# Kernel tuning notes

Hardware: AMD Instinct MI355X
Metric: run time of the kernel (lower is better)

## Reference

```python
import jax, jax.numpy as jnp
import numpy as np

EMBED, HEADS, LEVELS, POINTS, MLP = 256, 8, 3, 4, 4
SHAPES = [(60, 80), (30, 40), (15, 20)]  # (H, W) per level


def layer_norm(x, g, b):
    m = jnp.mean(x, -1, keepdims=True)
    v = jnp.mean((x - m) ** 2, -1, keepdims=True)
    return (x - m) * jax.lax.rsqrt(v + 1e-5) * g + b


def _bilinear(v, H, W, gx, gy):
    # v: [B,h,H*W,dh]; gx,gy: [B,h,Nq,P] absolute pixel coords (grid_sample align_corners=False, zero padding)
    x0 = jnp.floor(gx); y0 = jnp.floor(gy)
    wx = gx - x0; wy = gy - y0

    def g(xi, yi):
        valid = ((xi >= 0) & (xi < W) & (yi >= 0) & (yi < H)).astype(v.dtype)
        idx = jnp.clip(yi, 0, H - 1) * W + jnp.clip(xi, 0, W - 1)
        B, h, Nq, P = idx.shape
        out = jnp.take_along_axis(v, idx.reshape(B, h, Nq * P)[..., None], axis=2)
        return out.reshape(B, h, Nq, P, -1) * valid[..., None]

    x0i = x0.astype(jnp.int32); y0i = y0.astype(jnp.int32)
    return (g(x0i, y0i) * ((1 - wx) * (1 - wy))[..., None]
            + g(x0i + 1, y0i) * (wx * (1 - wy))[..., None]
            + g(x0i, y0i + 1) * ((1 - wx) * wy)[..., None]
            + g(x0i + 1, y0i + 1) * (wx * wy)[..., None])


def setup_inputs() -> dict:
    key = jax.random.key(0)
    ks = jax.random.split(key, 16)
    B, Nq, C = 2, 8192, EMBED
    Nv = sum(h * w for h, w in SHAPES)
    s = 0.02
    d = {
        'query': jax.random.normal(ks[0], (B, Nq, C), jnp.float32),
        'value': jax.random.normal(ks[1], (B, Nv, C), jnp.float32),
        'query_pos': jax.random.normal(ks[2], (B, Nq, C), jnp.float32),
        'ref_pts': jax.random.uniform(ks[3], (B, Nq, LEVELS, 2), jnp.float32),
        'spatial_shapes': jnp.array(SHAPES, jnp.int32),
        'level_start_index': jnp.array(np.cumsum([0] + [h * w for h, w in SHAPES[:-1]]), jnp.int32),
        'g1': jnp.ones((C,), jnp.float32), 'b1': jnp.zeros((C,), jnp.float32),
        'Wo': s * jax.random.normal(ks[4], (C, HEADS * LEVELS * POINTS * 2), jnp.float32),
        'bo': jnp.zeros((HEADS * LEVELS * POINTS * 2,), jnp.float32),
        'Wa': s * jax.random.normal(ks[5], (C, HEADS * LEVELS * POINTS), jnp.float32),
        'ba': jnp.zeros((HEADS * LEVELS * POINTS,), jnp.float32),
        'Wv': s * jax.random.normal(ks[6], (C, C), jnp.float32), 'bv': jnp.zeros((C,), jnp.float32),
        'Wp': s * jax.random.normal(ks[7], (C, C), jnp.float32), 'bp': jnp.zeros((C,), jnp.float32),
        'g2': jnp.ones((C,), jnp.float32), 'b2': jnp.zeros((C,), jnp.float32),
        'Wf1': s * jax.random.normal(ks[8], (C, MLP * C), jnp.float32), 'bf1': jnp.zeros((MLP * C,), jnp.float32),
        'Wf2': s * jax.random.normal(ks[9], (MLP * C, C), jnp.float32), 'bf2': jnp.zeros((C,), jnp.float32),
    }
    return d


def reference(query, value, query_pos, ref_pts, spatial_shapes, level_start_index,
              g1, b1, Wo, bo, Wa, ba, Wv, bv, Wp, bp, g2, b2, Wf1, bf1, Wf2, bf2):
    B, Nq, C = query.shape
    dh = C // HEADS
    shapes = np.asarray(spatial_shapes).tolist()
    starts = np.asarray(level_start_index).tolist()

    qn = layer_norm(query, g1, b1)           # pre-norm
    qa = qn + query_pos                       # positional embedding inside attn
    offs = (qa @ Wo + bo).reshape(B, Nq, HEADS, LEVELS, POINTS, 2)
    aw = jax.nn.softmax((qa @ Wa + ba).reshape(B, Nq, HEADS, LEVELS * POINTS), -1)
    aw = aw.reshape(B, Nq, HEADS, LEVELS, POINTS)
    v = (value @ Wv + bv).reshape(B, -1, HEADS, dh).transpose(0, 2, 1, 3)  # [B,h,Nv,dh]

    # offset_normalizer = (W, H) per level
    norm = jnp.array([[w, h] for h, w in shapes], jnp.float32)
    loc = ref_pts[:, :, None, :, None, :] + offs / norm[None, None, None, :, None, :]

    out = jnp.zeros((B, Nq, HEADS, dh), query.dtype)
    for l, (H, W) in enumerate(shapes):
        vl = jax.lax.dynamic_slice_in_dim(v, starts[l], H * W, axis=2)
        gl = loc[:, :, :, l].transpose(0, 2, 1, 3, 4)   # [B,h,Nq,P,2]
        gx = gl[..., 0] * W - 0.5
        gy = gl[..., 1] * H - 0.5
        sampled = _bilinear(vl, H, W, gx, gy)            # [B,h,Nq,P,dh]
        out = out + jnp.einsum('bhqpd,bqhp->bqhd', sampled, aw[:, :, :, l])

    attn = out.reshape(B, Nq, C) @ Wp + bp + qn          # output proj + mmcv internal residual (identity=norm1(query))
    q = query + attn                                     # layer residual
    q2 = layer_norm(q, g2, b2)
    return q + (jax.nn.gelu(q2 @ Wf1 + bf1, approximate=False) @ Wf2 + bf2)
```

## Files before the change

kernel.cpp:

```cpp
#include <hip/hip_runtime.h>
#include <math.h>


typedef short short8 __attribute__((ext_vector_type(8)));
typedef short s16x4 __attribute__((ext_vector_type(4)));
typedef __bf16 bf16x8 __attribute__((ext_vector_type(8)));
typedef float f32x4 __attribute__((ext_vector_type(4)));

__device__ __forceinline__ short f2b(float f) {
  unsigned u = __builtin_bit_cast(unsigned, f);
  u += 0x7fffu + ((u >> 16) & 1u);
  return (short)(u >> 16);
}
__device__ __forceinline__ float b2f(short s) {
  unsigned u = ((unsigned)(unsigned short)s) << 16;
  return __builtin_bit_cast(float, u);
}
__device__ __forceinline__ void b8f(short8 s, float* f) {
  const uint4 u = __builtin_bit_cast(uint4, s);
  f[0] = __builtin_bit_cast(float, u.x << 16);
  f[1] = __builtin_bit_cast(float, u.x & 0xffff0000u);
  f[2] = __builtin_bit_cast(float, u.y << 16);
  f[3] = __builtin_bit_cast(float, u.y & 0xffff0000u);
  f[4] = __builtin_bit_cast(float, u.z << 16);
  f[5] = __builtin_bit_cast(float, u.z & 0xffff0000u);
  f[6] = __builtin_bit_cast(float, u.w << 16);
  f[7] = __builtin_bit_cast(float, u.w & 0xffff0000u);
}

__device__ __forceinline__ f32x4 mfma16(short8 a, short8 b, f32x4 c) {
  return __builtin_amdgcn_mfma_f32_16x16x32_bf16(
      __builtin_bit_cast(bf16x8, a), __builtin_bit_cast(bf16x8, b), c, 0, 0, 0);
}

typedef __attribute__((address_space(3))) unsigned int lds_u32;
typedef const __attribute__((address_space(1))) unsigned int glb_u32;
__device__ __forceinline__ void glds16(const void* g, void* l) {
  __builtin_amdgcn_global_load_lds((glb_u32*)g, (lds_u32*)l, 16, 0, 0);
}

__device__ __forceinline__ float gelu1(float v) {
  return 0.5f * v * (1.f + erff(v * 0.70710678118654752f));
}

template <int EPI>
__device__ __forceinline__ void gemm64_core(
    int bx, int by,
    const short* __restrict__ A, const short* __restrict__ Bt,
    const float* __restrict__ bias, const float* __restrict__ bias2,
    const void* __restrict__ add1,
    void* __restrict__ Cout, int M, int Nreal, int ldc, int K, char* smem)
{
  short* sA = (short*)smem;
  short* sB = sA + 4096;
  float* sf = (float*)smem;

  const int t = threadIdx.x;
  const int wave = t >> 6, lane = t & 63;
  const int quad = lane >> 4, l16 = lane & 15;
  const int wm = (wave & 1) * 32, wn = (wave >> 1) * 64;
  const int m0 = by * 64, n0 = bx * 128;

  f32x4 acc[2][4];
#pragma unroll
  for (int i = 0; i < 2; i++)
#pragma unroll
    for (int j = 0; j < 4; j++) acc[i][j] = (f32x4){0.f, 0.f, 0.f, 0.f};

  const int srow = lane >> 3, pos = lane & 7;
  const int chunk = (pos + srow) & 7;
  const short* gA = A + (size_t)(m0 + wave * 16 + srow) * K + chunk * 8;
  const short* gB = Bt + (size_t)(n0 + wave * 32 + srow) * K + chunk * 8;

  const int nk = K >> 6;
  for (int kt = 0; kt < nk; ++kt) {
    if (kt) __syncthreads();
    const int ko = kt * 64;
#pragma unroll
    for (int g = 0; g < 2; ++g)
      glds16(gA + ko + (size_t)(g * 8) * K, sA + (wave * 16 + g * 8) * 64);
#pragma unroll
    for (int g = 0; g < 4; ++g)
      glds16(gB + ko + (size_t)(g * 8) * K, sB + (wave * 32 + g * 8) * 64);
    __syncthreads();
#pragma unroll
    for (int kk = 0; kk < 2; ++kk) {
      short8 af[2], bf[4];
      const int c = kk * 4 + quad;
#pragma unroll
      for (int i = 0; i < 2; i++) {
        const int lrA = wm + i * 16 + l16;
        af[i] = *(const short8*)&sA[lrA * 64 + ((c - lrA) & 7) * 8];
      }
#pragma unroll
      for (int j = 0; j < 4; j++) {
        const int lrB = wn + j * 16 + l16;
        bf[j] = *(const short8*)&sB[lrB * 64 + ((c - lrB) & 7) * 8];
      }
#pragma unroll
      for (int i = 0; i < 2; i++)
#pragma unroll
        for (int j = 0; j < 4; j++) acc[i][j] = mfma16(bf[j], af[i], acc[i][j]);
    }
  }
  __syncthreads();

#pragma unroll
  for (int b = 0; b < 2; ++b) {
    if (wm == b * 32) {
#pragma unroll
      for (int i = 0; i < 2; ++i) {
        const int rr = i * 16 + l16;
#pragma unroll
        for (int j = 0; j < 4; ++j)
          *(f32x4*)&sf[rr * 132 + wn + quad * 4 + j * 16] = acc[i][j];
      }
    }
    __syncthreads();
#pragma unroll
    for (int r2 = 0; r2 < 4; ++r2) {
      const int fidx = r2 * 1024 + t * 4;
      const int row = fidx >> 7, col = fidx & 127;
      const int gm = m0 + b * 32 + row;
      const int cc = n0 + col;
      if (gm < M && cc < Nreal) {
        const float4 v = *(const float4*)&sf[row * 132 + col];
        float4 bb;
        if (EPI == 4) bb = (cc < 192) ? *(const float4*)(bias + cc)
                                      : *(const float4*)(bias2 + cc - 192);
        else bb = *(const float4*)(bias + cc);
        float v0 = v.x + bb.x, v1 = v.y + bb.y, v2 = v.z + bb.z, v3 = v.w + bb.w;
        s16x4 o; o.x = f2b(v0); o.y = f2b(v1); o.z = f2b(v2); o.w = f2b(v3);
        *(s16x4*)((short*)Cout + (size_t)gm * ldc + cc) = o;
      }
    }
    __syncthreads();
  }
}

__global__ __launch_bounds__(256) void gemm_oa_v(
    const short* __restrict__ qa, const short* __restrict__ wt_oa,
    const float* __restrict__ bo, const float* __restrict__ ba,
    short* __restrict__ oabuf,
    const short* __restrict__ valbf, const short* __restrict__ wt_v,
    const float* __restrict__ bv, short* __restrict__ vproj)
{
  __shared__ __align__(16) char smem[24576];
  const int idx = blockIdx.x;
  if (idx < 768) {
    gemm64_core<4>(idx % 3, idx / 3, qa, wt_oa, bo, ba, nullptr,
                   oabuf, 16384, 288, 288, 256, smem);
  } else {
    const int r = idx - 768;
    gemm64_core<5>(r % 2, r / 2, valbf, wt_v, bv, nullptr, nullptr,
                   vproj, 12600, 256, 256, 256, smem);
  }
}

__global__ __launch_bounds__(256) void gemm_wp_ln2(
    const short* __restrict__ A, const short* __restrict__ Bt,
    const float* __restrict__ bias,
    const short* __restrict__ qnb, const float* __restrict__ query,
    const float* __restrict__ g2, const float* __restrict__ b2v,
    float* __restrict__ qbuf, short* __restrict__ q2)
{
  __shared__ __align__(16) char smem[36864];
  short* sA = (short*)smem;
  short* sB = sA + 2048;
  float* sf = (float*)smem;

  const int t = threadIdx.x;
  const int wave = t >> 6, lane = t & 63;
  const int quad = lane >> 4, l16 = lane & 15;
  const int wm = (wave & 1) * 16, wn = (wave >> 1) * 128;
  const int m0 = blockIdx.x * 32;
  const int K = 256;

  f32x4 acc[8];
#pragma unroll
  for (int j = 0; j < 8; j++) acc[j] = (f32x4){0.f, 0.f, 0.f, 0.f};

  const int srow = lane >> 3, pos = lane & 7;
  const int chunk = (pos + srow) & 7;
  const short* gA = A + (size_t)(m0 + wave * 8 + srow) * K + chunk * 8;
  const short* gB = Bt + (size_t)(wave * 64 + srow) * K + chunk * 8;

  for (int kt = 0; kt < 4; ++kt) {
    if (kt) __syncthreads();
    const int ko = kt * 64;
    glds16(gA + ko, sA + (wave * 8) * 64);
#pragma unroll
    for (int g = 0; g < 8; ++g)
      glds16(gB + ko + (size_t)(g * 8) * K, sB + (wave * 64 + g * 8) * 64);
    __syncthreads();
#pragma unroll
    for (int kk = 0; kk < 2; ++kk) {
      const int c = kk * 4 + quad;
      const int lrA = wm + l16;
      const short8 af = *(const short8*)&sA[lrA * 64 + ((c - lrA) & 7) * 8];
      short8 bf[8];
#pragma unroll
      for (int j = 0; j < 8; j++) {
        const int lrB = wn + j * 16 + l16;
        bf[j] = *(const short8*)&sB[lrB * 64 + ((c - lrB) & 7) * 8];
      }
#pragma unroll
      for (int j = 0; j < 8; j++) acc[j] = mfma16(bf[j], af, acc[j]);
    }
  }
  __syncthreads();

#pragma unroll
  for (int j = 0; j < 8; j++)
    *(f32x4*)&sf[(wm + l16) * 260 + wn + j * 16 + quad * 4] = acc[j];
  __syncthreads();

  const float4 bb   = *(const float4*)(bias + lane * 4);
  const float4 gv   = *(const float4*)(g2 + lane * 4);
  const float4 b2f4 = *(const float4*)(b2v + lane * 4);
#pragma unroll
  for (int rr = 0; rr < 8; ++rr) {
    const int row = wave * 8 + rr;
    const int gm = m0 + row;
    const float4 a = *(const float4*)&sf[row * 260 + lane * 4];
    const s16x4 qn = *(const s16x4*)(qnb + (size_t)gm * 256 + lane * 4);
    const float4 qv = *(const float4*)(query + (size_t)gm * 256 + lane * 4);
    float q0 = a.x + bb.x + b2f(qn.x) + qv.x;
    float q1 = a.y + bb.y + b2f(qn.y) + qv.y;
    float q2f = a.z + bb.z + b2f(qn.z) + qv.z;
    float q3 = a.w + bb.w + b2f(qn.w) + qv.w;
    float s = q0 + q1 + q2f + q3;
#pragma unroll
    for (int o = 32; o; o >>= 1) s += __shfl_xor(s, o);
    const float mean = s * (1.f / 256.f);
    const float d0 = q0 - mean, d1 = q1 - mean, d2 = q2f - mean, d3 = q3 - mean;
    float ss = d0 * d0 + d1 * d1 + d2 * d2 + d3 * d3;
#pragma unroll
    for (int o = 32; o; o >>= 1) ss += __shfl_xor(ss, o);
    const float inv = rsqrtf(ss * (1.f / 256.f) + 1e-5f);
    *(float4*)(qbuf + (size_t)gm * 256 + lane * 4) = make_float4(q0, q1, q2f, q3);
    s16x4 o2;
    o2.x = f2b(d0 * inv * gv.x + b2f4.x);
    o2.y = f2b(d1 * inv * gv.y + b2f4.y);
    o2.z = f2b(d2 * inv * gv.z + b2f4.z);
    o2.w = f2b(d3 * inv * gv.w + b2f4.w);
    *(s16x4*)(q2 + (size_t)gm * 256 + lane * 4) = o2;
  }
}

__global__ __launch_bounds__(1024, 4) void fused_mlp(
    const short* __restrict__ q2,
    const short* __restrict__ wf1,
    const float* __restrict__ b1v,
    const short* __restrict__ wf2,
    const float* __restrict__ b2v,
    const float* __restrict__ qbuf,
    float* __restrict__ outp)
{
  __shared__ __align__(16) char smem[147456];
  short* H  = (short*)smem;
  short* sA = (short*)(smem + 131072);
  float* sf = (float*)smem;

  const int t = threadIdx.x;
  const int w = t >> 6, lane = t & 63;
  const int quad = lane >> 4, l16 = lane & 15;
  const int m0 = blockIdx.x * 64;

  f32x4 acc[4][4];
#pragma unroll
  for (int i = 0; i < 4; i++)
#pragma unroll
    for (int j = 0; j < 4; j++) acc[i][j] = (f32x4){0.f, 0.f, 0.f, 0.f};

  for (int ap = 0; ap < 2; ++ap) {
    if (ap) __syncthreads();
    {
      const int row = t >> 4, pp = t & 15;
      const int cl = (pp & ~7) | ((pp + row) & 7);
      glds16(q2 + (size_t)(m0 + row) * 256 + (size_t)(ap * 16 + cl) * 8,
             sA + (size_t)w * 512);
    }
    __syncthreads();
#pragma unroll
    for (int kk = 0; kk < 4; ++kk) {
      const int cl = kk * 4 + quad;
      const int cg = ap * 16 + cl;
      short8 bfr[4], afr[4];
#pragma unroll
      for (int j = 0; j < 4; ++j) {
        const int n1 = w * 4 + j;
        bfr[j] = *(const short8*)(wf1 + ((size_t)n1 * 32 + cg) * 128 + l16 * 8);
      }
#pragma unroll
      for (int i = 0; i < 4; ++i) {
        const int r = i * 16 + l16;
        const int pos = (cl & ~7) | ((cl - r) & 7);
        afr[i] = *(const short8*)(sA + r * 128 + pos * 8);
      }
#pragma unroll
      for (int i = 0; i < 4; ++i)
#pragma unroll
        for (int j = 0; j < 4; ++j) acc[i][j] = mfma16(bfr[j], afr[i], acc[i][j]);
    }
  }
#pragma unroll
  for (int j = 0; j < 4; ++j) {
    const int colb = w * 64 + j * 16 + quad * 4;
    const float4 bb = *(const float4*)(b1v + colb);
    const int c = colb >> 3;
#pragma unroll
    for (int i = 0; i < 4; ++i) {
      const int r = i * 16 + l16;
      const int pos = (c & ~7) | ((c - r) & 7);
      s16x4 o;
      o.x = f2b(gelu1(acc[i][j].x + bb.x));
      o.y = f2b(gelu1(acc[i][j].y + bb.y));
      o.z = f2b(gelu1(acc[i][j].z + bb.z));
      o.w = f2b(gelu1(acc[i][j].w + bb.w));
      *(s16x4*)(H + r * 1024 + pos * 8 + (colb & 7)) = o;
    }
  }
  __syncthreads();

  float4 qv[4];
#pragma unroll
  for (int rep = 0; rep < 4; ++rep) {
    const int fidx = rep * 4096 + t * 4;
    qv[rep] = *(const float4*)(qbuf + (size_t)(m0 + (fidx >> 8)) * 256 + (fidx & 255));
  }

  const int wm2 = w >> 3, wn8 = w & 7;
  f32x4 acc2[2][2];
#pragma unroll
  for (int i = 0; i < 2; i++)
#pragma unroll
    for (int j = 0; j < 2; j++) acc2[i][j] = (f32x4){0.f, 0.f, 0.f, 0.f};

#pragma unroll 4
  for (int kk = 0; kk < 32; ++kk) {
    const int c = kk * 4 + quad;
    short8 bfr[2], afr[2];
#pragma unroll
    for (int j = 0; j < 2; ++j) {
      const int n1 = wn8 * 2 + j;
      bfr[j] = *(const short8*)(wf2 + ((size_t)n1 * 128 + c) * 128 + l16 * 8);
    }
#pragma unroll
    for (int i = 0; i < 2; ++i) {
      const int r = wm2 * 32 + i * 16 + l16;
      const int pos = (c & ~7) | ((c - r) & 7);
      afr[i] = *(const short8*)(H + r * 1024 + pos * 8);
    }
#pragma unroll
    for (int i = 0; i < 2; ++i)
#pragma unroll
      for (int j = 0; j < 2; ++j) acc2[i][j] = mfma16(bfr[j], afr[i], acc2[i][j]);
  }
  __syncthreads();

#pragma unroll
  for (int i = 0; i < 2; ++i)
#pragma unroll
    for (int j = 0; j < 2; ++j)
      *(f32x4*)&sf[(wm2 * 32 + i * 16 + l16) * 260 + wn8 * 32 + j * 16 + quad * 4] =
          acc2[i][j];
  __syncthreads();

#pragma unroll
  for (int rep = 0; rep < 4; ++rep) {
    const int fidx = rep * 4096 + t * 4;
    const int row = fidx >> 8, col = fidx & 255;
    const int gm = m0 + row;
    const float4 v  = *(const float4*)&sf[row * 260 + col];
    const float4 bb = *(const float4*)(b2v + col);
    *(float4*)(outp + (size_t)gm * 256 + col) =
        make_float4(v.x + bb.x + qv[rep].x, v.y + bb.y + qv[rep].y,
                    v.z + bb.z + qv[rep].z, v.w + bb.w + qv[rep].w);
  }
}

__global__ __launch_bounds__(256) void prep_all(
    const float* __restrict__ Wo, const float* __restrict__ Wa,
    const float* __restrict__ Wv, const float* __restrict__ Wp,
    const float* __restrict__ Wf1, const float* __restrict__ Wf2,
    short* __restrict__ t_oa, short* __restrict__ t_v, short* __restrict__ t_p,
    short* __restrict__ t_f1, short* __restrict__ t_f2,
    const float* __restrict__ value, short* __restrict__ valbf,
    const float* __restrict__ query, const float* __restrict__ query_pos,
    const float* __restrict__ g1, const float* __restrict__ b1,
    short* __restrict__ qnb, short* __restrict__ qa)
{
  __shared__ float tile[32][33];
  const int t = threadIdx.x;
  const int blk = blockIdx.x;

  if (blk < 1792) {
    const int bxa = blk & 255, bya = blk >> 8;
    int K, N, noff; const float* src; short* dst;
    switch (bya) {
      case 0: src = Wo;      dst = t_oa; K = 256;  N = 192;  noff = 0;   break;
      case 1: src = Wa;      dst = t_oa; K = 256;  N = 96;   noff = 192; break;
      case 2: src = nullptr; dst = t_oa; K = 256;  N = 96;   noff = 288; break;
      case 3: src = Wv;      dst = t_v;  K = 256;  N = 256;  noff = 0;   break;
      case 4: src = Wp;      dst = t_p;  K = 256;  N = 256;  noff = 0;   break;
      case 5: src = Wf1;     dst = t_f1; K = 256;  N = 1024; noff = 0;   break;
      default: src = Wf2;    dst = t_f2; K = 1024; N = 256;  noff = 0;   break;
    }
    const bool fragpack = (bya >= 5);
    const int tilesK = K >> 5;
    const int nt = tilesK * (N >> 5);
    if (bxa >= nt) return;
    const int tk = bxa % tilesK, tn = bxa / tilesK;
    const int k0 = tk * 32, n0 = tn * 32;
    const int r = t >> 3, c4 = (t & 7) * 4;
    float4 v = make_float4(0.f, 0.f, 0.f, 0.f);
    if (src) v = *(const float4*)(src + (size_t)(k0 + r) * N + n0 + c4);
    tile[r][c4] = v.x; tile[r][c4 + 1] = v.y; tile[r][c4 + 2] = v.z; tile[r][c4 + 3] = v.w;
    __syncthreads();
    const int nn = t >> 3, kc = (t & 7) * 4;
    s16x4 o;
    o.x = f2b(tile[kc][nn]); o.y = f2b(tile[kc + 1][nn]);
    o.z = f2b(tile[kc + 2][nn]); o.w = f2b(tile[kc + 3][nn]);
    if (fragpack) {
      const int n = n0 + nn, k = k0 + kc;
      *(s16x4*)(dst + ((size_t)(n >> 4) * (K >> 3) + (k >> 3)) * 128 +
                (n & 15) * 8 + (k & 7)) = o;
    } else {
      *(s16x4*)(dst + (size_t)(noff + n0 + nn) * K + k0 + kc) = o;
    }
  } else if (blk < 1792 + 3169) {
    const int i = ((blk - 1792) * 256 + t) * 4;
    if (i >= 12672 * 256) return;
    s16x4 o = (s16x4){0, 0, 0, 0};
    if (i < 12600 * 256) {
      float4 v = *(const float4*)(value + i);
      o.x = f2b(v.x); o.y = f2b(v.y); o.z = f2b(v.z); o.w = f2b(v.w);
    }
    *(s16x4*)(valbf + i) = o;
  } else {
    const int row  = (blk - 4961) * 4 + (t >> 6);
    const int lane = t & 63;
    const float4 v = ((const float4*)(query + (size_t)row * 256))[lane];
    float s = v.x + v.y + v.z + v.w;
#pragma unroll
    for (int o = 32; o; o >>= 1) s += __shfl_xor(s, o);
    const float mean = s * (1.f / 256.f);
    const float dx = v.x - mean, dy = v.y - mean, dz = v.z - mean, dw = v.w - mean;
    float s2 = dx * dx + dy * dy + dz * dz + dw * dw;
#pragma unroll
    for (int o = 32; o; o >>= 1) s2 += __shfl_xor(s2, o);
    const float inv = rsqrtf(s2 * (1.f / 256.f) + 1e-5f);
    const float4 gv = ((const float4*)g1)[lane];
    const float4 bv = ((const float4*)b1)[lane];
    const float4 o1 = make_float4(dx * inv * gv.x + bv.x, dy * inv * gv.y + bv.y,
                                  dz * inv * gv.z + bv.z, dw * inv * gv.w + bv.w);
    s16x4 ob; ob.x = f2b(o1.x); ob.y = f2b(o1.y); ob.z = f2b(o1.z); ob.w = f2b(o1.w);
    ((s16x4*)(qnb + (size_t)row * 256))[lane] = ob;
    const float4 pv = ((const float4*)(query_pos + (size_t)row * 256))[lane];
    s16x4 op;
    op.x = f2b(o1.x + pv.x); op.y = f2b(o1.y + pv.y);
    op.z = f2b(o1.z + pv.z); op.w = f2b(o1.w + pv.w);
    ((s16x4*)(qa + (size_t)row * 256))[lane] = op;
  }
}

__global__ __launch_bounds__(256) void deform_fused(
    const short* __restrict__ vproj, const short* __restrict__ oa,
    const float* __restrict__ refp, short* __restrict__ out)
{
  __shared__ int4 sIdx[768];
  __shared__ s16x4 sW[768];
  const int t = threadIdx.x;

  if (t < 64) {
    const int row = blockIdx.x * 8 + (t >> 3), h = t & 7;
    const short* oarow = oa + (size_t)row * 288;
    float off[24];
    {
      const short8* op = (const short8*)(oarow + h * 24);
      b8f(op[0], off); b8f(op[1], off + 8); b8f(op[2], off + 16);
    }
    float lg[12];
    {
      const s16x4* ap = (const s16x4*)(oarow + 192 + h * 12);
#pragma unroll
      for (int i = 0; i < 3; i++) {
        const s16x4 v = ap[i];
        lg[i * 4] = b2f(v.x); lg[i * 4 + 1] = b2f(v.y);
        lg[i * 4 + 2] = b2f(v.z); lg[i * 4 + 3] = b2f(v.w);
      }
    }
    const float* rp = refp + (size_t)row * 6;
    const float Rx[3] = {rp[0], rp[2], rp[4]}, Ry[3] = {rp[1], rp[3], rp[5]};
    float mx = lg[0];
#pragma unroll
    for (int i = 1; i < 12; i++) mx = fmaxf(mx, lg[i]);
    float sum = 0.f;
#pragma unroll
    for (int i = 0; i < 12; i++) { lg[i] = __expf(lg[i] - mx); sum += lg[i]; }
    const float inv = 1.f / sum;
    const int b = row >> 13;
    const int Hs[3] = {60, 30, 15}, Ws[3] = {80, 40, 20}, St[3] = {0, 4800, 6000};
#pragma unroll
    for (int p = 0; p < 12; p++) {
      const int l = p >> 2;
      const int W = Ws[l], H = Hs[l];
      const float gx = Rx[l] * W + off[p * 2]     - 0.5f;
      const float gy = Ry[l] * H + off[p * 2 + 1] - 0.5f;
      const float x0f = floorf(gx), y0f = floorf(gy);
      const float wx = gx - x0f, wy = gy - y0f;
      const int x0 = (int)x0f, y0 = (int)y0f;
      const float aw = lg[p] * inv;
      float cw[4] = {(1.f - wx) * (1.f - wy), wx * (1.f - wy),
                     (1.f - wx) * wy, wx * wy};
      const int base = b * 6300 + St[l];
      int ci[4];
#pragma unroll
      for (int k = 0; k < 4; k++) {
        const int xx = x0 + (k & 1), yy = y0 + (k >> 1);
        const bool valid = (xx >= 0) & (xx < W) & (yy >= 0) & (yy < H);
        const int xc = min(max(xx, 0), W - 1);
        const int yc = min(max(yy, 0), H - 1);
        ci[k] = ((base + yc * W + xc) << 8) + h * 32;
        cw[k] = valid ? cw[k] * aw : 0.f;
      }
      sIdx[t * 12 + p] = make_int4(ci[0], ci[1], ci[2], ci[3]);
      s16x4 wv; wv.x = f2b(cw[0]); wv.y = f2b(cw[1]); wv.z = f2b(cw[2]); wv.w = f2b(cw[3]);
      sW[t * 12 + p] = wv;
    }
  }
  __syncthreads();

  const int lu = t >> 2, c4 = (t & 3) * 8;
  float acc[8];
#pragma unroll
  for (int i = 0; i < 8; i++) acc[i] = 0.f;
#pragma unroll 2
  for (int p = 0; p < 12; p++) {
    const int4 idx = sIdx[lu * 12 + p];
    const s16x4 wb = sW[lu * 12 + p];
    const float w0 = b2f(wb.x), w1 = b2f(wb.y), w2 = b2f(wb.z), w3 = b2f(wb.w);
    const short8 v0 = *(const short8*)(vproj + idx.x + c4);
    const short8 v1 = *(const short8*)(vproj + idx.y + c4);
    const short8 v2 = *(const short8*)(vproj + idx.z + c4);
    const short8 v3 = *(const short8*)(vproj + idx.w + c4);
    float f0[8], f1[8], f2[8], f3[8];
    b8f(v0, f0); b8f(v1, f1); b8f(v2, f2); b8f(v3, f3);
#pragma unroll
    for (int j = 0; j < 8; j++)
      acc[j] += w0 * f0[j] + w1 * f1[j] + w2 * f2[j] + w3 * f3[j];
  }
  short8 o;
#pragma unroll
  for (int j = 0; j < 8; j++) o[j] = f2b(acc[j]);
  *(short8*)(out + (size_t)(blockIdx.x * 256 + t) * 8) = o;
}

extern "C" void kernel_launch(void* const* d_in, const int* in_sizes, int n_in,
                              void* d_out, int out_size, void* d_ws, size_t ws_size,
                              hipStream_t stream)
{
  const float* query     = (const float*)d_in[0];
  const float* value     = (const float*)d_in[1];
  const float* query_pos = (const float*)d_in[2];
  const float* ref_pts   = (const float*)d_in[3];
  const float* g1  = (const float*)d_in[6];
  const float* b1  = (const float*)d_in[7];
  const float* Wo  = (const float*)d_in[8];
  const float* bo  = (const float*)d_in[9];
  const float* Wa  = (const float*)d_in[10];
  const float* ba  = (const float*)d_in[11];
  const float* Wv  = (const float*)d_in[12];
  const float* bv  = (const float*)d_in[13];
  const float* Wp  = (const float*)d_in[14];
  const float* bp  = (const float*)d_in[15];
  const float* g2  = (const float*)d_in[16];
  const float* b2  = (const float*)d_in[17];
  const float* Wf1 = (const float*)d_in[18];
  const float* bf1 = (const float*)d_in[19];
  const float* Wf2 = (const float*)d_in[20];
  const float* bf2 = (const float*)d_in[21];

  char* ws = (char*)d_ws;
  short* wt_oa   = (short*)(ws + 0);
  short* wt_v    = (short*)(ws + 196608);
  short* wt_p    = (short*)(ws + 327680);
  short* wt_f1   = (short*)(ws + 458752);
  short* wt_f2   = (short*)(ws + 983040);
  short* qnb     = (short*)(ws + 1507328);
  short* qa      = (short*)(ws + 18284544);
  short* oabuf   = (short*)(ws + 26673152);
  short* vproj   = (short*)(ws + 45547520);
  short* sampled = (short*)(ws + 51998720);
  float* qbuf    = (float*)(ws + 60387328);
  short* valbf   = (short*)(ws + 77164544);
  short* q2      = qa;
  float* outp = (float*)d_out;

  prep_all<<<9057, 256, 0, stream>>>(Wo, Wa, Wv, Wp, Wf1, Wf2,
                                     wt_oa, wt_v, wt_p, wt_f1, wt_f2,
                                     value, valbf, query, query_pos,
                                     g1, b1, qnb, qa);
  gemm_oa_v<<<1162, 256, 0, stream>>>(qa, wt_oa, bo, ba, oabuf,
                                      valbf, wt_v, bv, vproj);
  deform_fused<<<2048, 256, 0, stream>>>(vproj, oabuf, ref_pts, sampled);
  gemm_wp_ln2<<<512, 256, 0, stream>>>(sampled, wt_p, bp, qnb, query,
                                       g2, b2, qbuf, q2);
  fused_mlp<<<256, 1024, 0, stream>>>(q2, wt_f1, bf1, wt_f2, bf2, qbuf, outp);
}
```

Measured before the change: 210.6 us.

## Fuse output projection and LayerNorm2 into the MLP kernel

Merges the Wp projection + residual + LayerNorm2 kernel into the fused MLP kernel, so the q2 and qbuf intermediates stay on chip (in LDS and registers) and are never written to or reread from global memory. The Wp weights are now fragment-packed so they can be read directly from global memory. The hidden layer is processed in two halves of 512 columns to shrink LDS use, which adds extra synchronisation and an inner loop. The 1024-thread blocks now also do the Wp GEMM, and that adds work per block.

Measured after the change: 207.5 us. Within noise of the previous version (-1.5%).

```diff
diff --git a/kernel.cpp b/kernel.cpp
--- a/kernel.cpp
+++ b/kernel.cpp
@@ -48,7 +48,6 @@
     int bx, int by,
     const short* __restrict__ A, const short* __restrict__ Bt,
     const float* __restrict__ bias, const float* __restrict__ bias2,
-    const void* __restrict__ add1,
     void* __restrict__ Cout, int M, int Nreal, int ldc, int K, char* smem)
 {
   short* sA = (short*)smem;
@@ -148,214 +147,194 @@
   __shared__ __align__(16) char smem[24576];
   const int idx = blockIdx.x;
   if (idx < 768) {
-    gemm64_core<4>(idx % 3, idx / 3, qa, wt_oa, bo, ba, nullptr,
+    gemm64_core<4>(idx % 3, idx / 3, qa, wt_oa, bo, ba,
                    oabuf, 16384, 288, 288, 256, smem);
   } else {
     const int r = idx - 768;
-    gemm64_core<5>(r % 2, r / 2, valbf, wt_v, bv, nullptr, nullptr,
+    gemm64_core<5>(r % 2, r / 2, valbf, wt_v, bv, nullptr,
                    vproj, 12600, 256, 256, 256, smem);
   }
 }
 
-__global__ __launch_bounds__(256) void gemm_wp_ln2(
-    const short* __restrict__ A, const short* __restrict__ Bt,
-    const float* __restrict__ bias,
-    const short* __restrict__ qnb, const float* __restrict__ query,
+__global__ __launch_bounds__(1024, 4) void wp_mlp(
+    const short* __restrict__ sampled,
+    const short* __restrict__ wtp,
+    const float* __restrict__ bp,
+    const short* __restrict__ qnb,
+    const float* __restrict__ query,
     const float* __restrict__ g2, const float* __restrict__ b2v,
-    float* __restrict__ qbuf, short* __restrict__ q2)
-{
-  __shared__ __align__(16) char smem[36864];
-  short* sA = (short*)smem;
-  short* sB = sA + 2048;
-  float* sf = (float*)smem;
-
-  const int t = threadIdx.x;
-  const int wave = t >> 6, lane = t & 63;
-  const int quad = lane >> 4, l16 = lane & 15;
-  const int wm = (wave & 1) * 16, wn = (wave >> 1) * 128;
-  const int m0 = blockIdx.x * 32;
-  const int K = 256;
-
-  f32x4 acc[8];
-#pragma unroll
-  for (int j = 0; j < 8; j++) acc[j] = (f32x4){0.f, 0.f, 0.f, 0.f};
-
-  const int srow = lane >> 3, pos = lane & 7;
-  const int chunk = (pos + srow) & 7;
-  const short* gA = A + (size_t)(m0 + wave * 8 + srow) * K + chunk * 8;
-  const short* gB = Bt + (size_t)(wave * 64 + srow) * K + chunk * 8;
-
-  for (int kt = 0; kt < 4; ++kt) {
-    if (kt) __syncthreads();
-    const int ko = kt * 64;
-    glds16(gA + ko, sA + (wave * 8) * 64);
-#pragma unroll
-    for (int g = 0; g < 8; ++g)
-      glds16(gB + ko + (size_t)(g * 8) * K, sB + (wave * 64 + g * 8) * 64);
-    __syncthreads();
-#pragma unroll
-    for (int kk = 0; kk < 2; ++kk) {
-      const int c = kk * 4 + quad;
-      const int lrA = wm + l16;
-      const short8 af = *(const short8*)&sA[lrA * 64 + ((c - lrA) & 7) * 8];
-      short8 bf[8];
-#pragma unroll
-      for (int j = 0; j < 8; j++) {
-        const int lrB = wn + j * 16 + l16;
-        bf[j] = *(const short8*)&sB[lrB * 64 + ((c - lrB) & 7) * 8];
-      }
-#pragma unroll
-      for (int j = 0; j < 8; j++) acc[j] = mfma16(bf[j], af, acc[j]);
-    }
-  }
-  __syncthreads();
-
-#pragma unroll
-  for (int j = 0; j < 8; j++)
-    *(f32x4*)&sf[(wm + l16) * 260 + wn + j * 16 + quad * 4] = acc[j];
-  __syncthreads();
-
-  const float4 bb   = *(const float4*)(bias + lane * 4);
-  const float4 gv   = *(const float4*)(g2 + lane * 4);
-  const float4 b2f4 = *(const float4*)(b2v + lane * 4);
-#pragma unroll
-  for (int rr = 0; rr < 8; ++rr) {
-    const int row = wave * 8 + rr;
-    const int gm = m0 + row;
-    const float4 a = *(const float4*)&sf[row * 260 + lane * 4];
-    const s16x4 qn = *(const s16x4*)(qnb + (size_t)gm * 256 + lane * 4);
-    const float4 qv = *(const float4*)(query + (size_t)gm * 256 + lane * 4);
-    float q0 = a.x + bb.x + b2f(qn.x) + qv.x;
-    float q1 = a.y + bb.y + b2f(qn.y) + qv.y;
-    float q2f = a.z + bb.z + b2f(qn.z) + qv.z;
-    float q3 = a.w + bb.w + b2f(qn.w) + qv.w;
-    float s = q0 + q1 + q2f + q3;
-#pragma unroll
-    for (int o = 32; o; o >>= 1) s += __shfl_xor(s, o);
-    const float mean = s * (1.f / 256.f);
-    const float d0 = q0 - mean, d1 = q1 - mean, d2 = q2f - mean, d3 = q3 - mean;
-    float ss = d0 * d0 + d1 * d1 + d2 * d2 + d3 * d3;
-#pragma unroll
-    for (int o = 32; o; o >>= 1) ss += __shfl_xor(ss, o);
-    const float inv = rsqrtf(ss * (1.f / 256.f) + 1e-5f);
-    *(float4*)(qbuf + (size_t)gm * 256 + lane * 4) = make_float4(q0, q1, q2f, q3);
-    s16x4 o2;
-    o2.x = f2b(d0 * inv * gv.x + b2f4.x);
-    o2.y = f2b(d1 * inv * gv.y + b2f4.y);
-    o2.z = f2b(d2 * inv * gv.z + b2f4.z);
-    o2.w = f2b(d3 * inv * gv.w + b2f4.w);
-    *(s16x4*)(q2 + (size_t)gm * 256 + lane * 4) = o2;
-  }
-}
-
-__global__ __launch_bounds__(1024, 4) void fused_mlp(
-    const short* __restrict__ q2,
     const short* __restrict__ wf1,
     const float* __restrict__ b1v,
     const short* __restrict__ wf2,
-    const float* __restrict__ b2v,
-    const float* __restrict__ qbuf,
+    const float* __restrict__ bf2v,
     float* __restrict__ outp)
 {
-  __shared__ __align__(16) char smem[147456];
+  __shared__ __align__(16) char smem[99328];
+  float* sf = (float*)smem;
   short* H  = (short*)smem;
-  short* sA = (short*)(smem + 131072);
-  float* sf = (float*)smem;
+  short* RA = (short*)(smem + 66560);
 
   const int t = threadIdx.x;
   const int w = t >> 6, lane = t & 63;
   const int quad = lane >> 4, l16 = lane & 15;
+  const int wm2 = w >> 3, wn8 = w & 7;
   const int m0 = blockIdx.x * 64;
 
-  f32x4 acc[4][4];
-#pragma unroll
-  for (int i = 0; i < 4; i++)
-#pragma unroll
-    for (int j = 0; j < 4; j++) acc[i][j] = (f32x4){0.f, 0.f, 0.f, 0.f};
-
-  for (int ap = 0; ap < 2; ++ap) {
-    if (ap) __syncthreads();
-    {
-      const int row = t >> 4, pp = t & 15;
-      const int cl = (pp & ~7) | ((pp + row) & 7);
-      glds16(q2 + (size_t)(m0 + row) * 256 + (size_t)(ap * 16 + cl) * 8,
-             sA + (size_t)w * 512);
-    }
-    __syncthreads();
-#pragma unroll
-    for (int kk = 0; kk < 4; ++kk) {
-      const int cl = kk * 4 + quad;
-      const int cg = ap * 16 + cl;
-      short8 bfr[4], afr[4];
-#pragma unroll
-      for (int j = 0; j < 4; ++j) {
-        const int n1 = w * 4 + j;
+#pragma unroll
+  for (int q = 0; q < 2; ++q) {
+    const int row = q * 32 + w * 2 + (lane >> 5);
+    const int pos = lane & 31;
+    const int cl = (pos & ~7) | ((pos + row) & 7);
+    glds16(sampled + (size_t)(m0 + row) * 256 + cl * 8, RA + q * 8192 + w * 512);
+  }
+  __syncthreads();
+
+  {
+    f32x4 accp[2][2];
+#pragma unroll
+    for (int i = 0; i < 2; i++)
+#pragma unroll
+      for (int j = 0; j < 2; j++) accp[i][j] = (f32x4){0.f, 0.f, 0.f, 0.f};
+#pragma unroll
+    for (int kk = 0; kk < 8; ++kk) {
+      const int c = kk * 4 + quad;
+      short8 bfr[2], afr[2];
+#pragma unroll
+      for (int j = 0; j < 2; ++j) {
+        const int n1 = wn8 * 2 + j;
+        bfr[j] = *(const short8*)(wtp + ((size_t)n1 * 32 + c) * 128 + l16 * 8);
+      }
+#pragma unroll
+      for (int i = 0; i < 2; ++i) {
+        const int r = wm2 * 32 + i * 16 + l16;
+        const int pos = (c & ~7) | ((c - r) & 7);
+        afr[i] = *(const short8*)(RA + r * 256 + pos * 8);
+      }
+#pragma unroll
+      for (int i = 0; i < 2; ++i)
+#pragma unroll
+        for (int j = 0; j < 2; ++j) accp[i][j] = mfma16(bfr[j], afr[i], accp[i][j]);
+    }
+#pragma unroll
+    for (int i = 0; i < 2; ++i)
+#pragma unroll
+      for (int j = 0; j < 2; ++j)
+        *(f32x4*)&sf[(wm2 * 32 + i * 16 + l16) * 260 + wn8 * 32 + j * 16 + quad * 4] =
+            accp[i][j];
+  }
+  __syncthreads();
+
+  float4 qb[4];
+  {
+    const float4 bbp  = *(const float4*)(bp + lane * 4);
+    const float4 gv   = *(const float4*)(g2 + lane * 4);
+    const float4 bb2  = *(const float4*)(b2v + lane * 4);
+#pragma unroll
+    for (int rep = 0; rep < 4; ++rep) {
+      const int row = rep * 16 + w;
+      const int gm = m0 + row;
+      const float4 a = *(const float4*)&sf[row * 260 + lane * 4];
+      const s16x4 qn = *(const s16x4*)(qnb + (size_t)gm * 256 + lane * 4);
+      const float4 qv = *(const float4*)(query + (size_t)gm * 256 + lane * 4);
+      float v0 = a.x + bbp.x + b2f(qn.x) + qv.x;
+      float v1 = a.y + bbp.y + b2f(qn.y) + qv.y;
+      float v2 = a.z + bbp.z + b2f(qn.z) + qv.z;
+      float v3 = a.w + bbp.w + b2f(qn.w) + qv.w;
+      float s = v0 + v1 + v2 + v3;
+#pragma unroll
+      for (int o = 32; o; o >>= 1) s += __shfl_xor(s, o);
+      const float mean = s * (1.f / 256.f);
+      const float d0 = v0 - mean, d1 = v1 - mean, d2 = v2 - mean, d3 = v3 - mean;
+      float ss = d0 * d0 + d1 * d1 + d2 * d2 + d3 * d3;
+#pragma unroll
+      for (int o = 32; o; o >>= 1) ss += __shfl_xor(ss, o);
+      const float inv = rsqrtf(ss * (1.f / 256.f) + 1e-5f);
+      qb[rep] = make_float4(v0, v1, v2, v3);
+      const int col = lane * 4;
+      const int c = col >> 3;
+      const int pos = (c & ~7) | ((c - row) & 7);
+      s16x4 o2;
+      o2.x = f2b(d0 * inv * gv.x + bb2.x);
+      o2.y = f2b(d1 * inv * gv.y + bb2.y);
+      o2.z = f2b(d2 * inv * gv.z + bb2.z);
+      o2.w = f2b(d3 * inv * gv.w + bb2.w);
+      *(s16x4*)(RA + row * 256 + pos * 8 + (col & 7)) = o2;
+    }
+  }
+  __syncthreads();
+
+  f32x4 acc2[2][2];
+#pragma unroll
+  for (int i = 0; i < 2; i++)
+#pragma unroll
+    for (int j = 0; j < 2; j++) acc2[i][j] = (f32x4){0.f, 0.f, 0.f, 0.f};
+
+  for (int h = 0; h < 2; ++h) {
+    if (h) __syncthreads();
+    f32x4 acc[4][2];
+#pragma unroll
+    for (int i = 0; i < 4; i++)
+#pragma unroll
+      for (int j = 0; j < 2; j++) acc[i][j] = (f32x4){0.f, 0.f, 0.f, 0.f};
+#pragma unroll
+    for (int kk = 0; kk < 8; ++kk) {
+      const int cg = kk * 4 + quad;
+      short8 bfr[2], afr[4];
+#pragma unroll
+      for (int j = 0; j < 2; ++j) {
+        const int n1 = h * 32 + w * 2 + j;
         bfr[j] = *(const short8*)(wf1 + ((size_t)n1 * 32 + cg) * 128 + l16 * 8);
       }
 #pragma unroll
       for (int i = 0; i < 4; ++i) {
         const int r = i * 16 + l16;
+        const int pos = (cg & ~7) | ((cg - r) & 7);
+        afr[i] = *(const short8*)(RA + r * 256 + pos * 8);
+      }
+#pragma unroll
+      for (int i = 0; i < 4; ++i)
+#pragma unroll
+        for (int j = 0; j < 2; ++j) acc[i][j] = mfma16(bfr[j], afr[i], acc[i][j]);
+    }
+#pragma unroll
+    for (int j = 0; j < 2; ++j) {
+      const int coll = (w * 2 + j) * 16 + quad * 4;
+      const float4 bb = *(const float4*)(b1v + h * 512 + coll);
+      const int c = coll >> 3;
+#pragma unroll
+      for (int i = 0; i < 4; ++i) {
+        const int r = i * 16 + l16;
+        const int pos = (c & ~7) | ((c - r) & 7);
+        s16x4 o;
+        o.x = f2b(gelu1(acc[i][j].x + bb.x));
+        o.y = f2b(gelu1(acc[i][j].y + bb.y));
+        o.z = f2b(gelu1(acc[i][j].z + bb.z));
+        o.w = f2b(gelu1(acc[i][j].w + bb.w));
+        *(s16x4*)(H + r * 512 + pos * 8 + (coll & 7)) = o;
+      }
+    }
+    __syncthreads();
+
+#pragma unroll 4
+    for (int kk = 0; kk < 16; ++kk) {
+      const int cl = kk * 4 + quad;
+      short8 bfr[2], afr[2];
+#pragma unroll
+      for (int j = 0; j < 2; ++j) {
+        const int n1 = wn8 * 2 + j;
+        bfr[j] = *(const short8*)(wf2 + ((size_t)n1 * 128 + h * 64 + cl) * 128 + l16 * 8);
+      }
+#pragma unroll
+      for (int i = 0; i < 2; ++i) {
+        const int r = wm2 * 32 + i * 16 + l16;
         const int pos = (cl & ~7) | ((cl - r) & 7);
-        afr[i] = *(const short8*)(sA + r * 128 + pos * 8);
-      }
-#pragma unroll
-      for (int i = 0; i < 4; ++i)
-#pragma unroll
-        for (int j = 0; j < 4; ++j) acc[i][j] = mfma16(bfr[j], afr[i], acc[i][j]);
-    }
-  }
-#pragma unroll
-  for (int j = 0; j < 4; ++j) {
-    const int colb = w * 64 + j * 16 + quad * 4;
-    const float4 bb = *(const float4*)(b1v + colb);
-    const int c = colb >> 3;
-#pragma unroll
-    for (int i = 0; i < 4; ++i) {
-      const int r = i * 16 + l16;
-      const int pos = (c & ~7) | ((c - r) & 7);
-      s16x4 o;
-      o.x = f2b(gelu1(acc[i][j].x + bb.x));
-      o.y = f2b(gelu1(acc[i][j].y + bb.y));
-      o.z = f2b(gelu1(acc[i][j].z + bb.z));
-      o.w = f2b(gelu1(acc[i][j].w + bb.w));
-      *(s16x4*)(H + r * 1024 + pos * 8 + (colb & 7)) = o;
-    }
-  }
-  __syncthreads();
-
-  float4 qv[4];
-#pragma unroll
-  for (int rep = 0; rep < 4; ++rep) {
-    const int fidx = rep * 4096 + t * 4;
-    qv[rep] = *(const float4*)(qbuf + (size_t)(m0 + (fidx >> 8)) * 256 + (fidx & 255));
-  }
-
-  const int wm2 = w >> 3, wn8 = w & 7;
-  f32x4 acc2[2][2];
-#pragma unroll
-  for (int i = 0; i < 2; i++)
-#pragma unroll
-    for (int j = 0; j < 2; j++) acc2[i][j] = (f32x4){0.f, 0.f, 0.f, 0.f};
-
-#pragma unroll 4
-  for (int kk = 0; kk < 32; ++kk) {
-    const int c = kk * 4 + quad;
-    short8 bfr[2], afr[2];
-#pragma unroll
-    for (int j = 0; j < 2; ++j) {
-      const int n1 = wn8 * 2 + j;
-      bfr[j] = *(const short8*)(wf2 + ((size_t)n1 * 128 + c) * 128 + l16 * 8);
-    }
-#pragma unroll
-    for (int i = 0; i < 2; ++i) {
-      const int r = wm2 * 32 + i * 16 + l16;
-      const int pos = (c & ~7) | ((c - r) & 7);
-      afr[i] = *(const short8*)(H + r * 1024 + pos * 8);
-    }
-#pragma unroll
-    for (int i = 0; i < 2; ++i)
-#pragma unroll
-      for (int j = 0; j < 2; ++j) acc2[i][j] = mfma16(bfr[j], afr[i], acc2[i][j]);
+        afr[i] = *(const short8*)(H + r * 512 + pos * 8);
+      }
+#pragma unroll
+      for (int i = 0; i < 2; ++i)
+#pragma unroll
+        for (int j = 0; j < 2; ++j) acc2[i][j] = mfma16(bfr[j], afr[i], acc2[i][j]);
+    }
   }
   __syncthreads();
 
@@ -367,16 +346,17 @@
           acc2[i][j];
   __syncthreads();
 
-#pragma unroll
-  for (int rep = 0; rep < 4; ++rep) {
-    const int fidx = rep * 4096 + t * 4;
-    const int row = fidx >> 8, col = fidx & 255;
-    const int gm = m0 + row;
-    const float4 v  = *(const float4*)&sf[row * 260 + col];
-    const float4 bb = *(const float4*)(b2v + col);
-    *(float4*)(outp + (size_t)gm * 256 + col) =
-        make_float4(v.x + bb.x + qv[rep].x, v.y + bb.y + qv[rep].y,
-                    v.z + bb.z + qv[rep].z, v.w + bb.w + qv[rep].w);
+  {
+    const float4 bbf = *(const float4*)(bf2v + lane * 4);
+#pragma unroll
+    for (int rep = 0; rep < 4; ++rep) {
+      const int row = rep * 16 + w;
+      const int gm = m0 + row;
+      const float4 v = *(const float4*)&sf[row * 260 + lane * 4];
+      *(float4*)(outp + (size_t)gm * 256 + lane * 4) =
+          make_float4(v.x + bbf.x + qb[rep].x, v.y + bbf.y + qb[rep].y,
+                      v.z + bbf.z + qb[rep].z, v.w + bbf.w + qb[rep].w);
+    }
   }
 }
 
@@ -407,7 +387,7 @@
       case 5: src = Wf1;     dst = t_f1; K = 256;  N = 1024; noff = 0;   break;
       default: src = Wf2;    dst = t_f2; K = 1024; N = 256;  noff = 0;   break;
     }
-    const bool fragpack = (bya >= 5);
+    const bool fragpack = (bya >= 4);
     const int tilesK = K >> 5;
     const int nt = tilesK * (N >> 5);
     if (bxa >= nt) return;
@@ -593,9 +573,7 @@
   short* oabuf   = (short*)(ws + 26673152);
   short* vproj   = (short*)(ws + 45547520);
   short* sampled = (short*)(ws + 51998720);
-  float* qbuf    = (float*)(ws + 60387328);
   short* valbf   = (short*)(ws + 77164544);
-  short* q2      = qa;
   float* outp = (float*)d_out;
 
   prep_all<<<9057, 256, 0, stream>>>(Wo, Wa, Wv, Wp, Wf1, Wf2,
@@ -605,7 +583,6 @@
   gemm_oa_v<<<1162, 256, 0, stream>>>(qa, wt_oa, bo, ba, oabuf,
                                       valbf, wt_v, bv, vproj);
   deform_fused<<<2048, 256, 0, stream>>>(vproj, oabuf, ref_pts, sampled);
-  gemm_wp_ln2<<<512, 256, 0, stream>>>(sampled, wt_p, bp, qnb, query,
-                                       g2, b2, qbuf, q2);
-  fused_mlp<<<256, 1024, 0, stream>>>(q2, wt_f1, bf1, wt_f2, bf2, qbuf, outp);
-}
+  wp_mlp<<<256, 1024, 0, stream>>>(sampled, wt_p, bp, qnb, query, g2, b2,
+                                   wt_f1, bf1, wt_f2, bf2, outp);
+}
```
